# Optimization experiments

Measured on AMD Instinct MI355X. Metric: run time of the kernel, lower is better.

Reference implementation:

```python
import jax, jax.numpy as jnp
import numpy as np

K, N = 4096, 4096
GROUP_SIZE = 128
N_GROUPS = N // GROUP_SIZE  # 32
B, S = 4, 2048
NBITS = 4


def setup_inputs() -> dict:
    key = jax.random.key(0)
    ks = jax.random.split(key, 7)
    x = jax.random.normal(ks[0], (B, S, N), dtype=jnp.float32)
    W_q = jax.random.randint(ks[1], (K, N), 0, 2 ** NBITS, dtype=jnp.int32)
    # positive per-group scales, zeros in quant range
    scales = jax.random.uniform(ks[2], (K, N_GROUPS, 1), dtype=jnp.float32, minval=0.005, maxval=0.05)
    zeros = jax.random.uniform(ks[3], (K, N_GROUPS, 1), dtype=jnp.float32, minval=0.0, maxval=float(2 ** NBITS - 1))
    mu1 = jax.random.uniform(ks[4], (N,), dtype=jnp.float32, minval=0.5, maxval=1.5)
    mu2 = jax.random.uniform(ks[5], (K,), dtype=jnp.float32, minval=0.5, maxval=1.5)
    bias = jax.random.normal(ks[6], (K,), dtype=jnp.float32)
    return {"x": x, "W_q": W_q, "scales": scales, "zeros": zeros, "mu1": mu1, "mu2": mu2, "bias": bias}


def reference(x, W_q, scales, zeros, mu1, mu2, bias):
    input_dtype = x.dtype
    n_groups = scales.shape[1]
    group_size = W_q.shape[1] // n_groups
    # group-wise dequant: (Q - zero) * scale
    Q_g = W_q.astype(jnp.float32).reshape(K, n_groups, group_size)
    W_deq_norm = (Q_g - zeros) * scales  # [K, n_groups, group_size]
    # mu1/mu2 rescale (inverse Sinkhorn normalization)
    W_deq = W_deq_norm.reshape(K, N) * mu2[:, None] * mu1[None, :]
    W_deq = W_deq.astype(input_dtype)
    # F.linear(x, W, b) = x @ W.T + b -> out [B, S, K]
    return jnp.einsum('bsn,kn->bsk', x, W_deq) + bias.astype(input_dtype)
```

## Files before the change

### kernel.cpp

```cpp
#include <hip/hip_runtime.h>
#include <hip/hip_bf16.h>
#include <stdint.h>

#define M_ROWS 8192
#define K_OUT  4096
#define N_RED  4096
#define NGRP   32
#define GROUP  128

#define BM 128
#define BN 128
#define BK 32

typedef __attribute__((ext_vector_type(8))) __bf16 bf16x8;
typedef __attribute__((ext_vector_type(4))) float   f32x4;


__device__ __forceinline__ unsigned short f32_to_bf16_rn(float f) {
  uint32_t u = __float_as_uint(f);
  uint32_t r = (u + 0x7FFFu + ((u >> 16) & 1u)) >> 16;
  return (unsigned short)r;
}

__device__ __forceinline__ void async_copy16(const void* gsrc, void* lds_base) {
  __builtin_amdgcn_global_load_lds(
      (const __attribute__((address_space(1))) uint32_t*)gsrc,
      (__attribute__((address_space(3))) uint32_t*)lds_base,
      16 , 0, 0);
}

__global__ __launch_bounds__(256) void cvt_x_kernel(
    const float* __restrict__ x, unsigned short* __restrict__ xb) {
  size_t idx = (size_t)blockIdx.x * 256 + threadIdx.x;
  const float4* xp = (const float4*)(x + idx * 8);
  float4 v0 = xp[0];
  float4 v1 = xp[1];
  union { unsigned short h[8]; uint4 v; } p;
  p.h[0] = f32_to_bf16_rn(v0.x);
  p.h[1] = f32_to_bf16_rn(v0.y);
  p.h[2] = f32_to_bf16_rn(v0.z);
  p.h[3] = f32_to_bf16_rn(v0.w);
  p.h[4] = f32_to_bf16_rn(v1.x);
  p.h[5] = f32_to_bf16_rn(v1.y);
  p.h[6] = f32_to_bf16_rn(v1.z);
  p.h[7] = f32_to_bf16_rn(v1.w);
  *(uint4*)(xb + idx * 8) = p.v;
}

__global__ __launch_bounds__(256) void dequant_w_kernel(
    const int* __restrict__ Wq, const float* __restrict__ scales,
    const float* __restrict__ zeros, const float* __restrict__ mu1,
    const float* __restrict__ mu2, unsigned short* __restrict__ Wb) {
  size_t idx = (size_t)blockIdx.x * 256 + threadIdx.x;
  int k = (int)(idx >> 9);
  int n = (int)(idx & 511) << 3;
  int g = n >> 7;
  float s  = scales[k * NGRP + g];
  float z  = zeros[k * NGRP + g];
  float sm = s * mu2[k];
  const int4* qp = (const int4*)(Wq + (size_t)k * N_RED + n);
  int4 q0 = qp[0];
  int4 q1 = qp[1];
  const float4* mp = (const float4*)(mu1 + n);
  float4 m0 = mp[0];
  float4 m1 = mp[1];
  union { unsigned short h[8]; uint4 v; } p;
  p.h[0] = f32_to_bf16_rn(((float)q0.x - z) * sm * m0.x);
  p.h[1] = f32_to_bf16_rn(((float)q0.y - z) * sm * m0.y);
  p.h[2] = f32_to_bf16_rn(((float)q0.z - z) * sm * m0.z);
  p.h[3] = f32_to_bf16_rn(((float)q0.w - z) * sm * m0.w);
  p.h[4] = f32_to_bf16_rn(((float)q1.x - z) * sm * m1.x);
  p.h[5] = f32_to_bf16_rn(((float)q1.y - z) * sm * m1.y);
  p.h[6] = f32_to_bf16_rn(((float)q1.z - z) * sm * m1.z);
  p.h[7] = f32_to_bf16_rn(((float)q1.w - z) * sm * m1.w);
  *(uint4*)(Wb + (size_t)k * N_RED + n) = p.v;
}

__global__ __launch_bounds__(256, 3) void gemm_bt_kernel(
    const unsigned short* __restrict__ A, const unsigned short* __restrict__ B,
    const float* __restrict__ bias, float* __restrict__ C) {
  __shared__ __align__(16) unsigned short As[BM * BK];
  __shared__ __align__(16) unsigned short Bs[BN * BK];

  int bid = blockIdx.x;
  int wg = (bid & 7) * 256 + (bid >> 3);
  int rowTile = wg >> 5;
  int colTile = wg & 31;

  int tid  = threadIdx.x;
  int wave = tid >> 6;
  int lane = tid & 63;
  int wr = wave >> 1;
  int wc = wave & 1;
  int fr = lane & 15;
  int fq = lane >> 4;

  int srow  = lane >> 2;
  int scol8 = (lane & 3) * 8;

  const unsigned short* Ag = A + (size_t)(rowTile * BM) * N_RED;
  const unsigned short* Bg = B + (size_t)(colTile * BN) * N_RED;

  f32x4 acc[4][4] = {};

  for (int kt = 0; kt < N_RED / BK; ++kt) {
    int kbase = kt * BK;
#pragma unroll
    for (int i = 0; i < 2; ++i) {
      int rbase = (i * 4 + wave) * 16;
      async_copy16(Ag + (size_t)(rbase + srow) * N_RED + kbase + scol8,
                   &As[rbase * BK]);
      async_copy16(Bg + (size_t)(rbase + srow) * N_RED + kbase + scol8,
                   &Bs[rbase * BK]);
    }
    __syncthreads();

    bf16x8 a[4], b[4];
#pragma unroll
    for (int m = 0; m < 4; ++m)
      a[m] = *(const bf16x8*)&As[(wr * 64 + m * 16 + fr) * BK + fq * 8];
#pragma unroll
    for (int n = 0; n < 4; ++n)
      b[n] = *(const bf16x8*)&Bs[(wc * 64 + n * 16 + fr) * BK + fq * 8];
#pragma unroll
    for (int m = 0; m < 4; ++m)
#pragma unroll
      for (int n = 0; n < 4; ++n)
        acc[m][n] =
            __builtin_amdgcn_mfma_f32_16x16x32_bf16(a[m], b[n], acc[m][n], 0, 0, 0);
    __syncthreads();
  }

  float bv[4];
#pragma unroll
  for (int n = 0; n < 4; ++n)
    bv[n] = bias[colTile * BN + wc * 64 + n * 16 + fr];
#pragma unroll
  for (int m = 0; m < 4; ++m) {
    int grow0 = rowTile * BM + wr * 64 + m * 16 + fq * 4;
#pragma unroll
    for (int j = 0; j < 4; ++j) {
      float* crow = C + (size_t)(grow0 + j) * K_OUT;
#pragma unroll
      for (int n = 0; n < 4; ++n)
        crow[colTile * BN + wc * 64 + n * 16 + fr] = acc[m][n][j] + bv[n];
    }
  }
}

extern "C" void kernel_launch(void* const* d_in, const int* in_sizes, int n_in,
                              void* d_out, int out_size, void* d_ws, size_t ws_size,
                              hipStream_t stream) {
  const float* x      = (const float*)d_in[0];
  const int*   Wq     = (const int*)d_in[1];
  const float* scales = (const float*)d_in[2];
  const float* zeros  = (const float*)d_in[3];
  const float* mu1    = (const float*)d_in[4];
  const float* mu2    = (const float*)d_in[5];
  const float* bias   = (const float*)d_in[6];
  float* out = (float*)d_out;

  unsigned short* xb = (unsigned short*)d_ws;
  unsigned short* Wb = (unsigned short*)((char*)d_ws +
                         (size_t)M_ROWS * N_RED * sizeof(unsigned short));

  cvt_x_kernel<<<(size_t)M_ROWS * N_RED / 8 / 256, 256, 0, stream>>>(x, xb);
  dequant_w_kernel<<<(size_t)K_OUT * N_RED / 8 / 256, 256, 0, stream>>>(
      Wq, scales, zeros, mu1, mu2, Wb);
  gemm_bt_kernel<<<(M_ROWS / BM) * (K_OUT / BN), 256, 0, stream>>>(xb, Wb, bias, out);
}
```

Before: 611.7 us.

## Rewrite GEMM with 256x256 tiles, double-buffered swizzled LDS, and merged prep kernel

Merges the x conversion and weight dequant into one grid-stride prep kernel, saving a launch. Replaces the 128x128x32 single-buffered GEMM with an 8-wave 256x256x64 kernel. The new kernel double-buffers LDS with async global-to-LDS loads, uses an XOR-swizzled LDS layout to avoid bank conflicts, and interleaves staged loads with MFMA blocks under explicit waitcnt and barriers. The larger tile raises arithmetic intensity and overlaps memory with compute. In exchange it uses 128KB of LDS per block, which lowers occupancy, and relies on fragile hand-written vmcnt scheduling.

Result: faster. 520.0 us (-15.0%).

```diff
diff --git a/kernel.cpp b/kernel.cpp
--- a/kernel.cpp
+++ b/kernel.cpp
@@ -6,11 +6,11 @@
 #define K_OUT  4096
 #define N_RED  4096
 #define NGRP   32
-#define GROUP  128
-
-#define BM 128
-#define BN 128
-#define BK 32
+
+#define BM 256
+#define BN 256
+#define BK 64
+#define NKT (N_RED / BK)
 
 typedef __attribute__((ext_vector_type(8))) __bf16 bf16x8;
 typedef __attribute__((ext_vector_type(4))) float   f32x4;
@@ -29,123 +29,198 @@
       16 , 0, 0);
 }
 
-__global__ __launch_bounds__(256) void cvt_x_kernel(
-    const float* __restrict__ x, unsigned short* __restrict__ xb) {
-  size_t idx = (size_t)blockIdx.x * 256 + threadIdx.x;
-  const float4* xp = (const float4*)(x + idx * 8);
-  float4 v0 = xp[0];
-  float4 v1 = xp[1];
-  union { unsigned short h[8]; uint4 v; } p;
-  p.h[0] = f32_to_bf16_rn(v0.x);
-  p.h[1] = f32_to_bf16_rn(v0.y);
-  p.h[2] = f32_to_bf16_rn(v0.z);
-  p.h[3] = f32_to_bf16_rn(v0.w);
-  p.h[4] = f32_to_bf16_rn(v1.x);
-  p.h[5] = f32_to_bf16_rn(v1.y);
-  p.h[6] = f32_to_bf16_rn(v1.z);
-  p.h[7] = f32_to_bf16_rn(v1.w);
-  *(uint4*)(xb + idx * 8) = p.v;
-}
-
-__global__ __launch_bounds__(256) void dequant_w_kernel(
-    const int* __restrict__ Wq, const float* __restrict__ scales,
-    const float* __restrict__ zeros, const float* __restrict__ mu1,
-    const float* __restrict__ mu2, unsigned short* __restrict__ Wb) {
-  size_t idx = (size_t)blockIdx.x * 256 + threadIdx.x;
-  int k = (int)(idx >> 9);
-  int n = (int)(idx & 511) << 3;
-  int g = n >> 7;
-  float s  = scales[k * NGRP + g];
-  float z  = zeros[k * NGRP + g];
-  float sm = s * mu2[k];
-  const int4* qp = (const int4*)(Wq + (size_t)k * N_RED + n);
-  int4 q0 = qp[0];
-  int4 q1 = qp[1];
-  const float4* mp = (const float4*)(mu1 + n);
-  float4 m0 = mp[0];
-  float4 m1 = mp[1];
-  union { unsigned short h[8]; uint4 v; } p;
-  p.h[0] = f32_to_bf16_rn(((float)q0.x - z) * sm * m0.x);
-  p.h[1] = f32_to_bf16_rn(((float)q0.y - z) * sm * m0.y);
-  p.h[2] = f32_to_bf16_rn(((float)q0.z - z) * sm * m0.z);
-  p.h[3] = f32_to_bf16_rn(((float)q0.w - z) * sm * m0.w);
-  p.h[4] = f32_to_bf16_rn(((float)q1.x - z) * sm * m1.x);
-  p.h[5] = f32_to_bf16_rn(((float)q1.y - z) * sm * m1.y);
-  p.h[6] = f32_to_bf16_rn(((float)q1.z - z) * sm * m1.z);
-  p.h[7] = f32_to_bf16_rn(((float)q1.w - z) * sm * m1.w);
-  *(uint4*)(Wb + (size_t)k * N_RED + n) = p.v;
-}
-
-__global__ __launch_bounds__(256, 3) void gemm_bt_kernel(
+constexpr size_t XCHUNKS = (size_t)M_ROWS * N_RED / 8;
+constexpr size_t WCHUNKS = (size_t)K_OUT * N_RED / 8;
+
+__global__ __launch_bounds__(256) void prep_kernel(
+    const float* __restrict__ x, const int* __restrict__ Wq,
+    const float* __restrict__ scales, const float* __restrict__ zeros,
+    const float* __restrict__ mu1, const float* __restrict__ mu2,
+    unsigned short* __restrict__ xb, unsigned short* __restrict__ Wb) {
+  const size_t stride = (size_t)gridDim.x * 256;
+  for (size_t c = (size_t)blockIdx.x * 256 + threadIdx.x;
+       c < XCHUNKS + WCHUNKS; c += stride) {
+    if (c < XCHUNKS) {
+      const float4* xp = (const float4*)(x + c * 8);
+      float4 v0 = xp[0];
+      float4 v1 = xp[1];
+      union { unsigned short h[8]; uint4 v; } p;
+      p.h[0] = f32_to_bf16_rn(v0.x); p.h[1] = f32_to_bf16_rn(v0.y);
+      p.h[2] = f32_to_bf16_rn(v0.z); p.h[3] = f32_to_bf16_rn(v0.w);
+      p.h[4] = f32_to_bf16_rn(v1.x); p.h[5] = f32_to_bf16_rn(v1.y);
+      p.h[6] = f32_to_bf16_rn(v1.z); p.h[7] = f32_to_bf16_rn(v1.w);
+      *(uint4*)(xb + c * 8) = p.v;
+    } else {
+      size_t idx = c - XCHUNKS;
+      int k = (int)(idx >> 9);
+      int n = (int)(idx & 511) << 3;
+      int g = n >> 7;
+      float s  = scales[k * NGRP + g];
+      float z  = zeros[k * NGRP + g];
+      float sm = s * mu2[k];
+      const int4* qp = (const int4*)(Wq + (size_t)k * N_RED + n);
+      int4 q0 = qp[0];
+      int4 q1 = qp[1];
+      const float4* mp = (const float4*)(mu1 + n);
+      float4 m0 = mp[0];
+      float4 m1 = mp[1];
+      union { unsigned short h[8]; uint4 v; } p;
+      p.h[0] = f32_to_bf16_rn(((float)q0.x - z) * sm * m0.x);
+      p.h[1] = f32_to_bf16_rn(((float)q0.y - z) * sm * m0.y);
+      p.h[2] = f32_to_bf16_rn(((float)q0.z - z) * sm * m0.z);
+      p.h[3] = f32_to_bf16_rn(((float)q0.w - z) * sm * m0.w);
+      p.h[4] = f32_to_bf16_rn(((float)q1.x - z) * sm * m1.x);
+      p.h[5] = f32_to_bf16_rn(((float)q1.y - z) * sm * m1.y);
+      p.h[6] = f32_to_bf16_rn(((float)q1.z - z) * sm * m1.z);
+      p.h[7] = f32_to_bf16_rn(((float)q1.w - z) * sm * m1.w);
+      *(uint4*)(Wb + (size_t)k * N_RED + n) = p.v;
+    }
+  }
+}
+
+__global__ __launch_bounds__(512, 2) void gemm8_kernel(
     const unsigned short* __restrict__ A, const unsigned short* __restrict__ B,
     const float* __restrict__ bias, float* __restrict__ C) {
-  __shared__ __align__(16) unsigned short As[BM * BK];
-  __shared__ __align__(16) unsigned short Bs[BN * BK];
-
-  int bid = blockIdx.x;
-  int wg = (bid & 7) * 256 + (bid >> 3);
-  int rowTile = wg >> 5;
-  int colTile = wg & 31;
-
-  int tid  = threadIdx.x;
-  int wave = tid >> 6;
-  int lane = tid & 63;
-  int wr = wave >> 1;
-  int wc = wave & 1;
-  int fr = lane & 15;
-  int fq = lane >> 4;
-
-  int srow  = lane >> 2;
-  int scol8 = (lane & 3) * 8;
-
-  const unsigned short* Ag = A + (size_t)(rowTile * BM) * N_RED;
-  const unsigned short* Bg = B + (size_t)(colTile * BN) * N_RED;
-
-  f32x4 acc[4][4] = {};
-
-  for (int kt = 0; kt < N_RED / BK; ++kt) {
-    int kbase = kt * BK;
-#pragma unroll
-    for (int i = 0; i < 2; ++i) {
-      int rbase = (i * 4 + wave) * 16;
-      async_copy16(Ag + (size_t)(rbase + srow) * N_RED + kbase + scol8,
-                   &As[rbase * BK]);
-      async_copy16(Bg + (size_t)(rbase + srow) * N_RED + kbase + scol8,
-                   &Bs[rbase * BK]);
+  __shared__ __align__(16) unsigned short lds[2][4][8192];
+
+  const int bid = blockIdx.x;
+  const int wg = (bid & 7) * 64 + (bid >> 3);
+  const int tileM = wg >> 4;
+  const int tileN = wg & 15;
+
+  const int tid  = threadIdx.x;
+  const int wave = tid >> 6;
+  const int lane = tid & 63;
+  const int wm = wave >> 2;
+  const int wn = wave & 3;
+  const int fr = lane & 15;
+  const int fq = lane >> 4;
+
+  const int laneoff =
+      (fr * 64 + fq * 16) ^ ((fr & 8) << 2) ^ ((fr & 4) << 2);
+
+  const unsigned short* srcA[2];
+  const unsigned short* srcB[2];
+#pragma unroll
+  for (int l = 0; l < 2; ++l) {
+    int a = (l * 512 + tid) * 16;
+    int q = a ^ (((a >> 9) & 1) << 5) ^ (((a >> 8) & 1) << 4);
+    int row = q >> 6;
+    int ce  = (q & 63) >> 1;
+    srcA[l] = A + (size_t)(tileM * BM + row) * N_RED + ce;
+    srcB[l] = B + (size_t)(tileN * BN + row) * N_RED + ce;
+  }
+  const int dst0 = wave * 512;
+  const int dst1 = 4096 + wave * 512;
+
+  f32x4 acc[8][4] = {};
+  bf16x8 af[8], bfr[2];
+
+#define STAGE(nb, h)                                                         \
+  do {                                                                       \
+    async_copy16(((h) & 1 ? srcB : srcA)[0] + ((h) >> 1) * 32,               \
+                 &lds[nb][h][dst0]);                                         \
+    async_copy16(((h) & 1 ? srcB : srcA)[1] + ((h) >> 1) * 32,               \
+                 &lds[nb][h][dst1]);                                         \
+  } while (0)
+
+#define READ_A(cb, ks)                                                       \
+  do {                                                                       \
+    const char* ab =                                                         \
+        (const char*)&lds[cb][(ks) * 2][0] + wm * 8192 + laneoff;            \
+    _Pragma("unroll") for (int m = 0; m < 8; ++m)                            \
+        af[m] = *(const bf16x8*)(ab + m * 1024);                             \
+  } while (0)
+
+#define READ_B(cb, ks, nh)                                                   \
+  do {                                                                       \
+    const char* bb_ = (const char*)&lds[cb][(ks) * 2 + 1][0] + wn * 4096 +   \
+                      laneoff + (nh) * 2048;                                 \
+    bfr[0] = *(const bf16x8*)(bb_);                                          \
+    bfr[1] = *(const bf16x8*)(bb_ + 1024);                                   \
+  } while (0)
+
+#define MFMA_BLK(nh)                                                         \
+  do {                                                                       \
+    __builtin_amdgcn_s_setprio(1);                                           \
+    _Pragma("unroll") for (int m = 0; m < 8; ++m) {                          \
+      acc[m][(nh) * 2] = __builtin_amdgcn_mfma_f32_16x16x32_bf16(            \
+          af[m], bfr[0], acc[m][(nh) * 2], 0, 0, 0);                         \
+      acc[m][(nh) * 2 + 1] = __builtin_amdgcn_mfma_f32_16x16x32_bf16(        \
+          af[m], bfr[1], acc[m][(nh) * 2 + 1], 0, 0, 0);                     \
+    }                                                                        \
+    __builtin_amdgcn_s_setprio(0);                                           \
+  } while (0)
+
+#pragma unroll
+  for (int h = 0; h < 4; ++h) STAGE(0, h);
+  srcA[0] += BK; srcA[1] += BK; srcB[0] += BK; srcB[1] += BK;
+
+  for (int t = 0; t < NKT - 1; ++t) {
+    const int cb = t & 1, nb = cb ^ 1;
+    asm volatile("s_waitcnt vmcnt(4)" ::: "memory");
+    __builtin_amdgcn_s_barrier();
+    __builtin_amdgcn_sched_barrier(0);
+    READ_A(cb, 0);
+    READ_B(cb, 0, 0);
+    STAGE(nb, 0);
+    MFMA_BLK(0);
+    __builtin_amdgcn_s_barrier();
+    __builtin_amdgcn_sched_barrier(0);
+    READ_B(cb, 0, 1);
+    STAGE(nb, 1);
+    MFMA_BLK(1);
+    asm volatile("s_waitcnt vmcnt(4)" ::: "memory");
+    __builtin_amdgcn_s_barrier();
+    __builtin_amdgcn_sched_barrier(0);
+    READ_A(cb, 1);
+    READ_B(cb, 1, 0);
+    STAGE(nb, 2);
+    MFMA_BLK(0);
+    __builtin_amdgcn_s_barrier();
+    __builtin_amdgcn_sched_barrier(0);
+    READ_B(cb, 1, 1);
+    STAGE(nb, 3);
+    MFMA_BLK(1);
+    srcA[0] += BK; srcA[1] += BK; srcB[0] += BK; srcB[1] += BK;
+  }
+  {
+    const int cb = (NKT - 1) & 1;
+    asm volatile("s_waitcnt vmcnt(4)" ::: "memory");
+    __builtin_amdgcn_s_barrier();
+    __builtin_amdgcn_sched_barrier(0);
+    READ_A(cb, 0); READ_B(cb, 0, 0); MFMA_BLK(0);
+    __builtin_amdgcn_s_barrier();
+    __builtin_amdgcn_sched_barrier(0);
+    READ_B(cb, 0, 1); MFMA_BLK(1);
+    asm volatile("s_waitcnt vmcnt(0)" ::: "memory");
+    __builtin_amdgcn_s_barrier();
+    __builtin_amdgcn_sched_barrier(0);
+    READ_A(cb, 1); READ_B(cb, 1, 0); MFMA_BLK(0);
+    __builtin_amdgcn_s_barrier();
+    __builtin_amdgcn_sched_barrier(0);
+    READ_B(cb, 1, 1); MFMA_BLK(1);
+  }
+
+  float bv[4];
+#pragma unroll
+  for (int n = 0; n < 4; ++n)
+    bv[n] = bias[tileN * BN + wn * 64 + n * 16 + fr];
+#pragma unroll
+  for (int m = 0; m < 8; ++m) {
+    int row0 = tileM * BM + wm * 128 + m * 16 + fq * 4;
+#pragma unroll
+    for (int j = 0; j < 4; ++j) {
+      float* crow = C + (size_t)(row0 + j) * K_OUT + tileN * BN + wn * 64 + fr;
+#pragma unroll
+      for (int n = 0; n < 4; ++n)
+        crow[n * 16] = acc[m][n][j] + bv[n];
     }
-    __syncthreads();
-
-    bf16x8 a[4], b[4];
-#pragma unroll
-    for (int m = 0; m < 4; ++m)
-      a[m] = *(const bf16x8*)&As[(wr * 64 + m * 16 + fr) * BK + fq * 8];
-#pragma unroll
-    for (int n = 0; n < 4; ++n)
-      b[n] = *(const bf16x8*)&Bs[(wc * 64 + n * 16 + fr) * BK + fq * 8];
-#pragma unroll
-    for (int m = 0; m < 4; ++m)
-#pragma unroll
-      for (int n = 0; n < 4; ++n)
-        acc[m][n] =
-            __builtin_amdgcn_mfma_f32_16x16x32_bf16(a[m], b[n], acc[m][n], 0, 0, 0);
-    __syncthreads();
-  }
-
-  float bv[4];
-#pragma unroll
-  for (int n = 0; n < 4; ++n)
-    bv[n] = bias[colTile * BN + wc * 64 + n * 16 + fr];
-#pragma unroll
-  for (int m = 0; m < 4; ++m) {
-    int grow0 = rowTile * BM + wr * 64 + m * 16 + fq * 4;
-#pragma unroll
-    for (int j = 0; j < 4; ++j) {
-      float* crow = C + (size_t)(grow0 + j) * K_OUT;
-#pragma unroll
-      for (int n = 0; n < 4; ++n)
-        crow[colTile * BN + wc * 64 + n * 16 + fr] = acc[m][n][j] + bv[n];
-    }
-  }
+  }
+#undef STAGE
+#undef READ_A
+#undef READ_B
+#undef MFMA_BLK
 }
 
 extern "C" void kernel_launch(void* const* d_in, const int* in_sizes, int n_in,
@@ -164,8 +239,6 @@
   unsigned short* Wb = (unsigned short*)((char*)d_ws +
                          (size_t)M_ROWS * N_RED * sizeof(unsigned short));
 
-  cvt_x_kernel<<<(size_t)M_ROWS * N_RED / 8 / 256, 256, 0, stream>>>(x, xb);
-  dequant_w_kernel<<<(size_t)K_OUT * N_RED / 8 / 256, 256, 0, stream>>>(
-      Wq, scales, zeros, mu1, mu2, Wb);
-  gemm_bt_kernel<<<(M_ROWS / BM) * (K_OUT / BN), 256, 0, stream>>>(xb, Wb, bias, out);
-}
+  prep_kernel<<<2048, 256, 0, stream>>>(x, Wq, scales, zeros, mu1, mu2, xb, Wb);
+  gemm8_kernel<<<(M_ROWS / BM) * (K_OUT / BN), 512, 0, stream>>>(xb, Wb, bias, out);
+}
```
